# Performance work log

Hardware: AMD Instinct MI355X
Metric: run time of the kernel (lower is better)

Reference implementation:

```python
import jax, jax.numpy as jnp
import numpy as np

N = 50000      # nodes
E = 800000     # edges
F = 128        # node feature dim (= output_size, residual)
H = 128        # hidden_size

def _uniform_fan_avg(key, shape):
    # VarianceScaling(scale=1.0, mode='fan_avg', distribution='uniform')
    fan_avg = (shape[0] + shape[1]) / 2.0
    limit = np.sqrt(3.0 / fan_avg)
    return jax.random.uniform(key, shape, jnp.float32, -limit, limit)

def setup_inputs() -> dict:
    key = jax.random.key(0)
    ks = jax.random.split(key, 16)
    h = jax.random.normal(ks[0], (N, F), jnp.float32)
    pos = jax.random.normal(ks[1], (N, 3), jnp.float32)
    senders = jax.random.randint(ks[2], (E,), 0, N, jnp.int32)
    receivers = jax.random.randint(ks[3], (E,), 0, N, jnp.int32)
    # edge_mlp: Linear(2F+1 -> H) silu, Linear(H -> H) silu (activate_final=True)
    eW1 = _uniform_fan_avg(ks[4], (2 * F + 1, H)); eb1 = jnp.zeros((H,), jnp.float32)
    eW2 = _uniform_fan_avg(ks[5], (H, H)); eb2 = jnp.zeros((H,), jnp.float32)
    # node_mlp: Linear(F+H -> H) silu, Linear(H -> F) (no final act)
    nW1 = _uniform_fan_avg(ks[6], (F + H, H)); nb1 = jnp.zeros((H,), jnp.float32)
    nW2 = _uniform_fan_avg(ks[7], (H, F)); nb2 = jnp.zeros((F,), jnp.float32)
    # pos_correction_mlp: Linear(H -> H) silu, Linear(H -> 1, no bias, UniformScaling(dt))
    pW1 = _uniform_fan_avg(ks[8], (H, H)); pb1 = jnp.zeros((H,), jnp.float32)
    dt = 0.001
    pW2 = jax.random.uniform(ks[9], (H, 1), jnp.float32, -dt, dt) * np.sqrt(3.0)
    return {"h": h, "pos": pos, "senders": senders, "receivers": receivers,
            "eW1": eW1, "eb1": eb1, "eW2": eW2, "eb2": eb2,
            "nW1": nW1, "nb1": nb1, "nW2": nW2, "nb2": nb2,
            "pW1": pW1, "pb1": pb1, "pW2": pW2}

def reference(h, pos, senders, receivers,
              eW1, eb1, eW2, eb2,
              nW1, nb1, nW2, nb2,
              pW1, pb1, pW2):
    n = h.shape[0]
    # _coord2radial (normalize=False)
    coord_diff = pos[senders] - pos[receivers]            # [E,3]
    radial = jnp.sum(coord_diff ** 2, axis=1, keepdims=True)  # [E,1]
    # edge update (_message): concat(h[senders], h[receivers], radial) -> edge_mlp
    msg_in = jnp.concatenate([h[senders], h[receivers], radial], axis=-1)  # [E,2F+1]
    msg = jax.nn.silu(msg_in @ eW1 + eb1)
    msg = jax.nn.silu(msg @ eW2 + eb2)                    # [E,H]
    # node update (_update): aggregate messages at receivers, node_mlp, residual
    agg = jax.ops.segment_sum(msg, receivers, num_segments=n)  # [N,H]
    x = jnp.concatenate([h, agg], axis=-1)                # [N,F+H]
    x = jax.nn.silu(x @ nW1 + nb1)
    x = x @ nW2 + nb2                                     # [N,F]
    h_new = h + x                                         # residual
    # position update (_pos_update)
    pc = jax.nn.silu(msg @ pW1 + pb1) @ pW2               # [E,1]
    trans = jnp.clip(coord_diff * pc, -100, 100)          # [E,3]
    pos_new = pos + jax.ops.segment_sum(trans, senders, num_segments=n)
    return h_new, pos_new
```

## Files before the change

### kernel.cpp

```cpp
#include <hip/hip_runtime.h>
#include <hip/hip_bf16.h>

#define NNODES 50000
#define NEDGES 800000
#define EB 1024
#define SCAN_BLOCKS 196
#define TRN_BLOCKS 448

typedef short bf16x8 __attribute__((ext_vector_type(8)));
typedef float f32x4 __attribute__((ext_vector_type(4)));
typedef unsigned short u16;
typedef unsigned int u32;

__device__ __forceinline__ u16 f2bf(float f) {
    __hip_bfloat16 b = __float2bfloat16(f);
    return *reinterpret_cast<u16*>(&b);
}
__device__ __forceinline__ float bf2f(u16 v) {
    u32 u = ((u32)v) << 16;
    return __uint_as_float(u);
}
__device__ __forceinline__ u32 pack2(float a, float b) {
    __hip_bfloat162 t = __float22bfloat162_rn(float2{a, b});
    return *reinterpret_cast<u32*>(&t);
}
__device__ __forceinline__ float fast_silu(float x) {
    float e = __builtin_amdgcn_exp2f(-1.442695040888963f * x);
    return x * __builtin_amdgcn_rcpf(1.0f + e);
}
__device__ __forceinline__ bf16x8 ld8(const u16* p) {
    return *(const bf16x8*)p;
}
__device__ __forceinline__ f32x4 mfma16(bf16x8 a, bf16x8 b, f32x4 c) {
    return __builtin_amdgcn_mfma_f32_16x16x32_bf16(a, b, c, 0, 0, 0);
}
__device__ __forceinline__ void bar_lds() {
    asm volatile("s_waitcnt lgkmcnt(0)\n\ts_barrier" ::: "memory");
}

__global__ void prep_kernel(const float* __restrict__ eW1, const float* __restrict__ eW2,
                            const float* __restrict__ pW1, const float* __restrict__ nW1,
                            const float* __restrict__ nW2,
                            u16* __restrict__ eW1T, u16* __restrict__ eW2T,
                            u16* __restrict__ pW1T, u16* __restrict__ nW1T,
                            u16* __restrict__ nW2T,
                            const int* __restrict__ rcv, int* __restrict__ counts) {
    int b = blockIdx.x;
    if (b < TRN_BLOCKS) {
        int i = b * 256 + threadIdx.x;
        const float* src; u16* dst; int K;
        if (i < 32768)      { src = eW1; dst = eW1T; K = 256; }
        else if (i < 49152) { src = eW2; dst = eW2T; K = 128; i -= 32768; }
        else if (i < 65536) { src = pW1; dst = pW1T; K = 128; i -= 49152; }
        else if (i < 98304) { src = nW1; dst = nW1T; K = 256; i -= 65536; }
        else                { src = nW2; dst = nW2T; K = 128; i -= 98304; }
        int n = i / K, k = i - n * K;
        dst[i] = f2bf(src[k * 128 + n]);
    } else {
        int e = (b - TRN_BLOCKS) * 256 + threadIdx.x;
        if (e < NEDGES) atomicAdd(&counts[rcv[e]], 1);
    }
}

__global__ __launch_bounds__(256) void gemm_p(
    const float* __restrict__ h, const u16* __restrict__ eW1T,
    const u16* __restrict__ nW1T, const float* __restrict__ eb1,
    u16* __restrict__ P)
{
    const int tid  = threadIdx.x;
    const int w    = tid >> 6;
    const int lane = tid & 63;
    const int m    = lane & 15;
    const int quad = lane >> 4;
    const int ksub = quad * 8;

    bf16x8 bw[4][6];
    float bias[6];
    #pragma unroll
    for (int cc = 0; cc < 6; cc++) {
        int C = 96 * w + 16 * cc + m;
        const u16* bp;
        if (C < 128)      { bp = eW1T + C * 256;               bias[cc] = 0.5f * eb1[C]; }
        else if (C < 256) { bp = eW1T + (C - 128) * 256 + 128; bias[cc] = 0.5f * eb1[C - 128]; }
        else              { bp = nW1T + (C - 256) * 256;       bias[cc] = 0.f; }
        #pragma unroll
        for (int t = 0; t < 4; t++) bw[t][cc] = ld8(bp + t * 32 + ksub);
    }
    const int base = blockIdx.x * 64;
    #pragma unroll
    for (int mt = 0; mt < 4; mt++) {
        int nm = base + mt * 16 + m;
        if (nm >= NNODES) nm = NNODES - 1;
        bf16x8 afr[4];
        #pragma unroll
        for (int t = 0; t < 4; t++) {
            const float* ap = h + (size_t)nm * 128 + t * 32 + ksub;
            f32x4 lo = *(const f32x4*)ap;
            f32x4 hi = *(const f32x4*)(ap + 4);
            #pragma unroll
            for (int j = 0; j < 4; j++) {
                afr[t][j]     = (short)f2bf(lo[j]);
                afr[t][4 + j] = (short)f2bf(hi[j]);
            }
        }
        f32x4 acc[6];
        #pragma unroll
        for (int cc = 0; cc < 6; cc++) acc[cc] = (f32x4){0,0,0,0};
        #pragma unroll
        for (int t = 0; t < 4; t++)
            #pragma unroll
            for (int cc = 0; cc < 6; cc++)
                acc[cc] = mfma16(afr[t], bw[t][cc], acc[cc]);
        #pragma unroll
        for (int cc = 0; cc < 6; cc++) {
            int C = 96 * w + 16 * cc + m;
            #pragma unroll
            for (int r = 0; r < 4; r++) {
                int nr = base + mt * 16 + quad * 4 + r;
                if (nr < NNODES) P[(size_t)nr * 384 + C] = f2bf(acc[cc][r] + bias[cc]);
            }
        }
    }
}

__global__ void scan1(const int* __restrict__ counts, int* __restrict__ excl,
                      int* __restrict__ blkSum) {
    __shared__ int tmp[256];
    int tx = threadIdx.x;
    int i = blockIdx.x * 256 + tx;
    int v = (i < NNODES) ? counts[i] : 0;
    tmp[tx] = v;
    __syncthreads();
    for (int off = 1; off < 256; off <<= 1) {
        int t = (tx >= off) ? tmp[tx - off] : 0;
        __syncthreads();
        tmp[tx] += t;
        __syncthreads();
    }
    if (i < NNODES) excl[i] = tmp[tx] - v;
    if (tx == 255) blkSum[blockIdx.x] = tmp[255];
}
__global__ void scan2(const int* __restrict__ blkSum, int* __restrict__ blkOff) {
    __shared__ int tmp[256];
    int tx = threadIdx.x;
    int v = (tx < SCAN_BLOCKS) ? blkSum[tx] : 0;
    tmp[tx] = v;
    __syncthreads();
    for (int off = 1; off < 256; off <<= 1) {
        int t = (tx >= off) ? tmp[tx - off] : 0;
        __syncthreads();
        tmp[tx] += t;
        __syncthreads();
    }
    if (tx < SCAN_BLOCKS) blkOff[tx] = tmp[tx] - v;
}
__global__ void scan3(const int* __restrict__ excl, const int* __restrict__ blkOff,
                      int* __restrict__ cursor) {
    int i = blockIdx.x * 256 + threadIdx.x;
    if (i < NNODES) cursor[i] = excl[i] + blkOff[blockIdx.x];
}
__global__ void scatter_kernel(const int* __restrict__ rcv, int* __restrict__ cursor,
                               int* __restrict__ perm) {
    int e = blockIdx.x * 256 + threadIdx.x;
    if (e < NEDGES) {
        int p = atomicAdd(&cursor[rcv[e]], 1);
        perm[p] = e;
    }
}

struct __align__(16) EdgeLds {
    u16   m1[64 * 136];
    u16   msg[64 * 136];
    float diff[64][4];
    float pcpart[4][64];
    float wlast[128];
    int   sndloc[64];
    int   rcvloc[64];
    unsigned long long bmap;
};

__global__ __launch_bounds__(256, 4) void edge_kernel(
    const u16* __restrict__ P, const float* __restrict__ pos,
    const int* __restrict__ snd, const int* __restrict__ rcv,
    const int* __restrict__ perm,
    const float* __restrict__ eW1last,
    const u16* __restrict__ eW2T, const float* __restrict__ eb2,
    const u16* __restrict__ pW1T, const float* __restrict__ pb1,
    const float* __restrict__ pW2,
    float* __restrict__ agg, float* __restrict__ posacc)
{
    __shared__ EdgeLds S;
    const int tid  = threadIdx.x;
    const int w    = tid >> 6;
    const int lane = tid & 63;
    const int m    = lane & 15;
    const int quad = lane >> 4;
    const int ksub = quad * 8;

    bf16x8 bw2[4][2], bp1[4][2];
    float b2v[2], pb1v[2], pw2v[2];
    #pragma unroll
    for (int cc = 0; cc < 2; cc++) {
        int col = (2 * w + cc) * 16 + m;
        #pragma unroll
        for (int t = 0; t < 4; t++) {
            bw2[t][cc] = ld8(eW2T + col * 128 + t * 32 + ksub);
            bp1[t][cc] = ld8(pW1T + col * 128 + t * 32 + ksub);
        }
        b2v[cc]  = eb2[col];
        pb1v[cc] = pb1[col];
        pw2v[cc] = pW2[col];
    }
    if (tid < 128) S.wlast[tid] = eW1last[tid];

    const int NT  = NEDGES / 64;
    const int xcd = blockIdx.x & 7;
    const int ib  = blockIdx.x >> 3;
    const int per = (NT + 7) / 8;
    const int t0  = xcd * per;
    const int t1  = (t0 + per < NT) ? t0 + per : NT;

    int eg_n = 0, s_n = 0, r_n = 0;
    if (t0 + ib < t1) {
        eg_n = perm[(t0 + ib) * 64 + lane];
        s_n = snd[eg_n]; r_n = rcv[eg_n];
    }

    for (int t = t0 + ib; t < t1; t += 128) {
        const int s = s_n, r = r_n;
        const int tn = t + 128;
        const int tp = (tn < t1) ? tn : t;
        int eg2 = perm[tp * 64 + lane];

        float d0 = pos[s * 3 + 0] - pos[r * 3 + 0];
        float d1 = pos[s * 3 + 1] - pos[r * 3 + 1];
        float d2 = pos[s * 3 + 2] - pos[r * 3 + 2];
        float rad = d0 * d0 + d1 * d1 + d2 * d2;

        bar_lds();
        if (tid < 64) {
            S.sndloc[tid] = s; S.rcvloc[tid] = r;
            S.diff[tid][0] = d0; S.diff[tid][1] = d1; S.diff[tid][2] = d2;
            int pv = __shfl_up(r, 1);
            unsigned long long bm = __ballot(lane > 0 && r != pv);
            if (tid == 0) S.bmap = bm;
        }
        {
            const int sw = lane >> 3;
            const u16* pa = P + (size_t)s * 384 + w * 32;
            const u16* pb = P + (size_t)r * 384 + 128 + w * 32;
            #pragma unroll
            for (int k = 0; k < 4; k++) {
                bf16x8 va = ld8(pa + k * 8);
                bf16x8 vb = ld8(pb + k * 8);
                u32 pk[4];
                #pragma unroll
                for (int jj = 0; jj < 4; jj++) {
                    int col = w * 32 + k * 8 + jj * 2;
                    float2 wl = *(const float2*)&S.wlast[col];
                    float v0 = bf2f((u16)va[jj * 2])     + bf2f((u16)vb[jj * 2])     + rad * wl.x;
                    float v1 = bf2f((u16)va[jj * 2 + 1]) + bf2f((u16)vb[jj * 2 + 1]) + rad * wl.y;
                    pk[jj] = pack2(fast_silu(v0), fast_silu(v1));
                }
                int chunk = (w * 4 + k) ^ sw;
                *(uint4*)&S.m1[lane * 136 + chunk * 8] =
                    make_uint4(pk[0], pk[1], pk[2], pk[3]);
            }
        }
        s_n = snd[eg2]; r_n = rcv[eg2]; eg_n = eg2;

        bar_lds();
        #pragma unroll
        for (int mt = 0; mt < 4; mt++) {
            const int rs = mt * 2 + (m >> 3);
            const int row = mt * 16 + m;
            f32x4 acc0 = (f32x4){0,0,0,0}, acc1 = (f32x4){0,0,0,0};
            #pragma unroll
            for (int t4 = 0; t4 < 4; t4++) {
                bf16x8 a = *(const bf16x8*)&S.m1[row * 136 + ((t4 * 4 + quad) ^ rs) * 8];
                acc0 = mfma16(a, bw2[t4][0], acc0);
                acc1 = mfma16(a, bw2[t4][1], acc1);
            }
            #pragma unroll
            for (int cc = 0; cc < 2; cc++) {
                f32x4 acc = cc ? acc1 : acc0;
                int col = (2 * w + cc) * 16 + m;
                #pragma unroll
                for (int rr = 0; rr < 4; rr++) {
                    int orow = mt * 16 + quad * 4 + rr;
                    S.msg[orow * 136 + col] = f2bf(fast_silu(acc[rr] + b2v[cc]));
                }
            }
        }
        bar_lds();
        #pragma unroll
        for (int mt = 0; mt < 4; mt++) {
            f32x4 acc0 = (f32x4){0,0,0,0}, acc1 = (f32x4){0,0,0,0};
            #pragma unroll
            for (int t4 = 0; t4 < 4; t4++) {
                bf16x8 a = *(const bf16x8*)&S.msg[(mt * 16 + m) * 136 + t4 * 32 + ksub];
                acc0 = mfma16(a, bp1[t4][0], acc0);
                acc1 = mfma16(a, bp1[t4][1], acc1);
            }
            float p4[4];
            #pragma unroll
            for (int rr = 0; rr < 4; rr++)
                p4[rr] = fast_silu(acc0[rr] + pb1v[0]) * pw2v[0]
                       + fast_silu(acc1[rr] + pb1v[1]) * pw2v[1];
            #pragma unroll
            for (int mask = 1; mask < 16; mask <<= 1) {
                #pragma unroll
                for (int rr = 0; rr < 4; rr++) p4[rr] += __shfl_xor(p4[rr], mask);
            }
            if (m == 0) {
                #pragma unroll
                for (int rr = 0; rr < 4; rr++)
                    S.pcpart[w][mt * 16 + quad * 4 + rr] = p4[rr];
            }
        }
        {
            int half = tid >> 7, col = tid & 127;
            int r0 = half * 32;
            u32 bm32 = __builtin_amdgcn_readfirstlane((u32)(S.bmap >> r0)) & ~1u;
            float a = 0.f;
            int cur = S.rcvloc[r0];
            int rr = r0;
            const int end0 = r0 + 32;
            while (true) {
                int nb = bm32 ? (r0 + __builtin_ctz(bm32)) : end0;
                for (; rr < nb; ++rr) a += bf2f(S.msg[rr * 136 + col]);
                atomicAdd(&agg[(size_t)cur * 128 + col], a);
                if (nb == end0) break;
                a = 0.f;
                cur = S.rcvloc[nb];
                bm32 &= bm32 - 1;
            }
        }
        bar_lds();
        if (tid < 192) {
            int ee = tid / 3, c = tid - ee * 3;
            float pc = S.pcpart[0][ee] + S.pcpart[1][ee] + S.pcpart[2][ee] + S.pcpart[3][ee];
            float tr = S.diff[ee][c] * pc;
            tr = fminf(fmaxf(tr, -100.f), 100.f);
            atomicAdd(&posacc[S.sndloc[ee] * 3 + c], tr);
        }
    }
}

__global__ __launch_bounds__(256, 4) void node_kernel(
    const u16* __restrict__ P, const float* __restrict__ h,
    const float* __restrict__ agg,
    const u16* __restrict__ nW1T, const float* __restrict__ nb1,
    const u16* __restrict__ nW2T, const float* __restrict__ nb2,
    const float* __restrict__ pos, const float* __restrict__ posacc,
    float* __restrict__ out)
{
    __shared__ alignas(16) u16 m1[64 * 136];
    const int tid  = threadIdx.x;
    const int w    = tid >> 6;
    const int lane = tid & 63;
    const int m    = lane & 15;
    const int quad = lane >> 4;
    const int ksub = quad * 8;

    bf16x8 bw1[4][2], bw2[4][2];
    float b1v[2], b2v[2];
    #pragma unroll
    for (int cc = 0; cc < 2; cc++) {
        int col = (2 * w + cc) * 16 + m;
        #pragma unroll
        for (int t = 0; t < 4; t++) {
            bw1[t][cc] = ld8(nW1T + col * 256 + 128 + t * 32 + ksub);
            bw2[t][cc] = ld8(nW2T + col * 128 + t * 32 + ksub);
        }
        b1v[cc] = nb1[col];
        b2v[cc] = nb2[col];
    }
    const int base = blockIdx.x * 64;
    #pragma unroll
    for (int mt = 0; mt < 4; mt++) {
        int nm = base + mt * 16 + m;
        if (nm >= NNODES) nm = NNODES - 1;
        f32x4 acc0 = (f32x4){0,0,0,0}, acc1 = (f32x4){0,0,0,0};
        #pragma unroll
        for (int t = 0; t < 4; t++) {
            const float* ap = agg + (size_t)nm * 128 + t * 32 + ksub;
            f32x4 lo = *(const f32x4*)ap;
            f32x4 hi = *(const f32x4*)(ap + 4);
            bf16x8 a;
            #pragma unroll
            for (int j = 0; j < 4; j++) {
                a[j]     = (short)f2bf(lo[j]);
                a[4 + j] = (short)f2bf(hi[j]);
            }
            acc0 = mfma16(a, bw1[t][0], acc0);
            acc1 = mfma16(a, bw1[t][1], acc1);
        }
        #pragma unroll
        for (int cc = 0; cc < 2; cc++) {
            f32x4 acc = cc ? acc1 : acc0;
            int col = (2 * w + cc) * 16 + m;
            #pragma unroll
            for (int rr = 0; rr < 4; rr++) {
                int row = mt * 16 + quad * 4 + rr;
                int nrc = base + row; if (nrc >= NNODES) nrc = NNODES - 1;
                float v = acc[rr] + bf2f(P[(size_t)nrc * 384 + 256 + col]) + b1v[cc];
                m1[row * 136 + col] = f2bf(fast_silu(v));
            }
        }
    }
    __syncthreads();
    #pragma unroll
    for (int mt = 0; mt < 4; mt++) {
        f32x4 acc0 = (f32x4){0,0,0,0}, acc1 = (f32x4){0,0,0,0};
        #pragma unroll
        for (int t = 0; t < 4; t++) {
            bf16x8 a = *(const bf16x8*)&m1[(mt * 16 + m) * 136 + t * 32 + ksub];
            acc0 = mfma16(a, bw2[t][0], acc0);
            acc1 = mfma16(a, bw2[t][1], acc1);
        }
        #pragma unroll
        for (int cc = 0; cc < 2; cc++) {
            f32x4 acc = cc ? acc1 : acc0;
            int col = (2 * w + cc) * 16 + m;
            #pragma unroll
            for (int rr = 0; rr < 4; rr++) {
                int nr = base + mt * 16 + quad * 4 + rr;
                if (nr < NNODES)
                    out[(size_t)nr * 128 + col] = acc[rr] + b2v[cc] + h[(size_t)nr * 128 + col];
            }
        }
    }
    if (tid < 192) {
        int i = blockIdx.x * 192 + tid;
        if (i < NNODES * 3) out[NNODES * 128 + i] = pos[i] + posacc[i];
    }
}

extern "C" void kernel_launch(void* const* d_in, const int* in_sizes, int n_in,
                              void* d_out, int out_size, void* d_ws, size_t ws_size,
                              hipStream_t stream) {
    (void)in_sizes; (void)n_in; (void)out_size; (void)ws_size;
    const float* h   = (const float*)d_in[0];
    const float* pos = (const float*)d_in[1];
    const int*   snd = (const int*)d_in[2];
    const int*   rcv = (const int*)d_in[3];
    const float* eW1 = (const float*)d_in[4];
    const float* eb1 = (const float*)d_in[5];
    const float* eW2 = (const float*)d_in[6];
    const float* eb2 = (const float*)d_in[7];
    const float* nW1 = (const float*)d_in[8];
    const float* nb1 = (const float*)d_in[9];
    const float* nW2 = (const float*)d_in[10];
    const float* nb2 = (const float*)d_in[11];
    const float* pW1 = (const float*)d_in[12];
    const float* pb1 = (const float*)d_in[13];
    const float* pW2 = (const float*)d_in[14];
    float* out = (float*)d_out;

    float* agg    = (float*)d_ws;
    float* posacc = agg + (size_t)NNODES * 128;
    u16* P    = (u16*)(posacc + (size_t)NNODES * 3);
    u16* eW1T = P + (size_t)NNODES * 384;
    u16* eW2T = eW1T + 128 * 256;
    u16* pW1T = eW2T + 128 * 128;
    u16* nW1T = pW1T + 128 * 128;
    u16* nW2T = nW1T + 128 * 256;
    int* counts = (int*)(nW2T + 128 * 128);
    int* excl   = counts + 50048;
    int* blkSum = excl + 50048;
    int* blkOff = blkSum + 256;
    int* cursor = blkOff + 256;
    int* perm   = cursor + 50048;

    hipMemsetAsync(agg, 0, (size_t)NNODES * 131 * sizeof(float), stream);
    hipMemsetAsync(counts, 0, 50048 * sizeof(int), stream);

    prep_kernel<<<TRN_BLOCKS + (NEDGES + 255) / 256, 256, 0, stream>>>(
        eW1, eW2, pW1, nW1, nW2, eW1T, eW2T, pW1T, nW1T, nW2T, rcv, counts);

    gemm_p<<<(NNODES + 63) / 64, 256, 0, stream>>>(h, eW1T, nW1T, eb1, P);

    scan1<<<SCAN_BLOCKS, 256, 0, stream>>>(counts, excl, blkSum);
    scan2<<<1, 256, 0, stream>>>(blkSum, blkOff);
    scan3<<<SCAN_BLOCKS, 256, 0, stream>>>(excl, blkOff, cursor);
    scatter_kernel<<<(NEDGES + 255) / 256, 256, 0, stream>>>(rcv, cursor, perm);

    edge_kernel<<<EB, 256, 0, stream>>>(
        P, pos, snd, rcv, perm,
        eW1 + 256 * 128,
        eW2T, eb2, pW1T, pb1, pW2,
        agg, posacc);

    node_kernel<<<(NNODES + 63) / 64, 256, 0, stream>>>(
        P, h, agg, nW1T, nb1, nW2T, nb2, pos, posacc, out);
}
```

Before: 454.9 us.

## Swap MFMA operand order for packed msg stores and fold scan3 into scatter

```diff
diff --git a/kernel.cpp b/kernel.cpp
--- a/kernel.cpp
+++ b/kernel.cpp
@@ -154,16 +154,13 @@
     }
     if (tx < SCAN_BLOCKS) blkOff[tx] = tmp[tx] - v;
 }
-__global__ void scan3(const int* __restrict__ excl, const int* __restrict__ blkOff,
-                      int* __restrict__ cursor) {
-    int i = blockIdx.x * 256 + threadIdx.x;
-    if (i < NNODES) cursor[i] = excl[i] + blkOff[blockIdx.x];
-}
-__global__ void scatter_kernel(const int* __restrict__ rcv, int* __restrict__ cursor,
+__global__ void scatter_kernel(const int* __restrict__ rcv, const int* __restrict__ excl,
+                               const int* __restrict__ blkOff, int* __restrict__ delta,
                                int* __restrict__ perm) {
     int e = blockIdx.x * 256 + threadIdx.x;
     if (e < NEDGES) {
-        int p = atomicAdd(&cursor[rcv[e]], 1);
+        int r = rcv[e];
+        int p = excl[r] + blkOff[r >> 8] + atomicAdd(&delta[r], 1);
         perm[p] = e;
     }
 }
@@ -174,6 +171,9 @@
     float diff[64][4];
     float pcpart[4][64];
     float wlast[128];
+    float eb2s[128];
+    float pb1s[128];
+    float pw2s[128];
     int   sndloc[64];
     int   rcvloc[64];
     unsigned long long bmap;
@@ -198,7 +198,6 @@
     const int ksub = quad * 8;
 
     bf16x8 bw2[4][2], bp1[4][2];
-    float b2v[2], pb1v[2], pw2v[2];
     #pragma unroll
     for (int cc = 0; cc < 2; cc++) {
         int col = (2 * w + cc) * 16 + m;
@@ -207,11 +206,13 @@
             bw2[t][cc] = ld8(eW2T + col * 128 + t * 32 + ksub);
             bp1[t][cc] = ld8(pW1T + col * 128 + t * 32 + ksub);
         }
-        b2v[cc]  = eb2[col];
-        pb1v[cc] = pb1[col];
-        pw2v[cc] = pW2[col];
-    }
-    if (tid < 128) S.wlast[tid] = eW1last[tid];
+    }
+    if (tid < 128) {
+        S.wlast[tid] = eW1last[tid];
+        S.eb2s[tid]  = eb2[tid];
+        S.pb1s[tid]  = pb1[tid];
+        S.pw2s[tid]  = pW2[tid];
+    }
 
     const int NT  = NEDGES / 64;
     const int xcd = blockIdx.x & 7;
@@ -240,19 +241,20 @@
         bar_lds();
         if (tid < 64) {
             S.sndloc[tid] = s; S.rcvloc[tid] = r;
-            S.diff[tid][0] = d0; S.diff[tid][1] = d1; S.diff[tid][2] = d2;
+            S.diff[tid][0] = d0; S.diff[tid][1] = d1;
+            S.diff[tid][2] = d2; S.diff[tid][3] = 0.f;
             int pv = __shfl_up(r, 1);
             unsigned long long bm = __ballot(lane > 0 && r != pv);
             if (tid == 0) S.bmap = bm;
         }
         {
             const int sw = lane >> 3;
-            const u16* pa = P + (size_t)s * 384 + w * 32;
-            const u16* pb = P + (size_t)r * 384 + 128 + w * 32;
+            const u16* pap = P + (size_t)s * 384 + w * 32;
+            const u16* pbp = P + (size_t)r * 384 + 128 + w * 32;
             #pragma unroll
             for (int k = 0; k < 4; k++) {
-                bf16x8 va = ld8(pa + k * 8);
-                bf16x8 vb = ld8(pb + k * 8);
+                bf16x8 va = ld8(pap + k * 8);
+                bf16x8 vb = ld8(pbp + k * 8);
                 u32 pk[4];
                 #pragma unroll
                 for (int jj = 0; jj < 4; jj++) {
@@ -270,52 +272,52 @@
         s_n = snd[eg2]; r_n = rcv[eg2]; eg_n = eg2;
 
         bar_lds();
-        #pragma unroll
-        for (int mt = 0; mt < 4; mt++) {
-            const int rs = mt * 2 + (m >> 3);
-            const int row = mt * 16 + m;
-            f32x4 acc0 = (f32x4){0,0,0,0}, acc1 = (f32x4){0,0,0,0};
-            #pragma unroll
-            for (int t4 = 0; t4 < 4; t4++) {
-                bf16x8 a = *(const bf16x8*)&S.m1[row * 136 + ((t4 * 4 + quad) ^ rs) * 8];
-                acc0 = mfma16(a, bw2[t4][0], acc0);
-                acc1 = mfma16(a, bw2[t4][1], acc1);
-            }
-            #pragma unroll
-            for (int cc = 0; cc < 2; cc++) {
-                f32x4 acc = cc ? acc1 : acc0;
-                int col = (2 * w + cc) * 16 + m;
+        {
+            f32x4 b2a = *(const f32x4*)&S.eb2s[(2 * w + 0) * 16 + quad * 4];
+            f32x4 b2b = *(const f32x4*)&S.eb2s[(2 * w + 1) * 16 + quad * 4];
+            #pragma unroll
+            for (int mt = 0; mt < 4; mt++) {
+                const int rs = mt * 2 + (m >> 3);
+                const int row = mt * 16 + m;
+                f32x4 acc0 = (f32x4){0,0,0,0}, acc1 = (f32x4){0,0,0,0};
                 #pragma unroll
-                for (int rr = 0; rr < 4; rr++) {
-                    int orow = mt * 16 + quad * 4 + rr;
-                    S.msg[orow * 136 + col] = f2bf(fast_silu(acc[rr] + b2v[cc]));
+                for (int t4 = 0; t4 < 4; t4++) {
+                    bf16x8 a = *(const bf16x8*)&S.m1[row * 136 + ((t4 * 4 + quad) ^ rs) * 8];
+                    acc0 = mfma16(bw2[t4][0], a, acc0);
+                    acc1 = mfma16(bw2[t4][1], a, acc1);
                 }
+                u32 q0 = pack2(fast_silu(acc0[0] + b2a[0]), fast_silu(acc0[1] + b2a[1]));
+                u32 q1 = pack2(fast_silu(acc0[2] + b2a[2]), fast_silu(acc0[3] + b2a[3]));
+                u32 q2 = pack2(fast_silu(acc1[0] + b2b[0]), fast_silu(acc1[1] + b2b[1]));
+                u32 q3 = pack2(fast_silu(acc1[2] + b2b[2]), fast_silu(acc1[3] + b2b[3]));
+                *(uint2*)&S.msg[row * 136 + (2 * w + 0) * 16 + quad * 4] = make_uint2(q0, q1);
+                *(uint2*)&S.msg[row * 136 + (2 * w + 1) * 16 + quad * 4] = make_uint2(q2, q3);
             }
         }
         bar_lds();
-        #pragma unroll
-        for (int mt = 0; mt < 4; mt++) {
-            f32x4 acc0 = (f32x4){0,0,0,0}, acc1 = (f32x4){0,0,0,0};
-            #pragma unroll
-            for (int t4 = 0; t4 < 4; t4++) {
-                bf16x8 a = *(const bf16x8*)&S.msg[(mt * 16 + m) * 136 + t4 * 32 + ksub];
-                acc0 = mfma16(a, bp1[t4][0], acc0);
-                acc1 = mfma16(a, bp1[t4][1], acc1);
-            }
-            float p4[4];
-            #pragma unroll
-            for (int rr = 0; rr < 4; rr++)
-                p4[rr] = fast_silu(acc0[rr] + pb1v[0]) * pw2v[0]
-                       + fast_silu(acc1[rr] + pb1v[1]) * pw2v[1];
-            #pragma unroll
-            for (int mask = 1; mask < 16; mask <<= 1) {
+        {
+            f32x4 p1a = *(const f32x4*)&S.pb1s[(2 * w + 0) * 16 + quad * 4];
+            f32x4 p1b = *(const f32x4*)&S.pb1s[(2 * w + 1) * 16 + quad * 4];
+            f32x4 w2a = *(const f32x4*)&S.pw2s[(2 * w + 0) * 16 + quad * 4];
+            f32x4 w2b = *(const f32x4*)&S.pw2s[(2 * w + 1) * 16 + quad * 4];
+            #pragma unroll
+            for (int mt = 0; mt < 4; mt++) {
+                const int row = mt * 16 + m;
+                f32x4 acc0 = (f32x4){0,0,0,0}, acc1 = (f32x4){0,0,0,0};
                 #pragma unroll
-                for (int rr = 0; rr < 4; rr++) p4[rr] += __shfl_xor(p4[rr], mask);
-            }
-            if (m == 0) {
+                for (int t4 = 0; t4 < 4; t4++) {
+                    bf16x8 a = *(const bf16x8*)&S.msg[row * 136 + t4 * 32 + ksub];
+                    acc0 = mfma16(bp1[t4][0], a, acc0);
+                    acc1 = mfma16(bp1[t4][1], a, acc1);
+                }
+                float part = 0.f;
                 #pragma unroll
                 for (int rr = 0; rr < 4; rr++)
-                    S.pcpart[w][mt * 16 + quad * 4 + rr] = p4[rr];
+                    part += fast_silu(acc0[rr] + p1a[rr]) * w2a[rr]
+                          + fast_silu(acc1[rr] + p1b[rr]) * w2b[rr];
+                part += __shfl_xor(part, 16);
+                part += __shfl_xor(part, 32);
+                if (quad == 0) S.pcpart[w][mt * 16 + m] = part;
             }
         }
         {
@@ -467,14 +469,14 @@
     u16* nW1T = pW1T + 128 * 128;
     u16* nW2T = nW1T + 128 * 256;
     int* counts = (int*)(nW2T + 128 * 128);
-    int* excl   = counts + 50048;
+    int* delta  = counts + 50048;
+    int* excl   = delta + 50048;
     int* blkSum = excl + 50048;
     int* blkOff = blkSum + 256;
-    int* cursor = blkOff + 256;
-    int* perm   = cursor + 50048;
+    int* perm   = blkOff + 256;
 
     hipMemsetAsync(agg, 0, (size_t)NNODES * 131 * sizeof(float), stream);
-    hipMemsetAsync(counts, 0, 50048 * sizeof(int), stream);
+    hipMemsetAsync(counts, 0, 2 * 50048 * sizeof(int), stream);
 
     prep_kernel<<<TRN_BLOCKS + (NEDGES + 255) / 256, 256, 0, stream>>>(
         eW1, eW2, pW1, nW1, nW2, eW1T, eW2T, pW1T, nW1T, nW2T, rcv, counts);
@@ -483,8 +485,8 @@
 
     scan1<<<SCAN_BLOCKS, 256, 0, stream>>>(counts, excl, blkSum);
     scan2<<<1, 256, 0, stream>>>(blkSum, blkOff);
-    scan3<<<SCAN_BLOCKS, 256, 0, stream>>>(excl, blkOff, cursor);
-    scatter_kernel<<<(NEDGES + 255) / 256, 256, 0, stream>>>(rcv, cursor, perm);
+    scatter_kernel<<<(NEDGES + 255) / 256, 256, 0, stream>>>(
+        rcv, excl, blkOff, delta, perm);
 
     edge_kernel<<<EB, 256, 0, stream>>>(
         P, pos, snd, rcv, perm,
```

After: 460.1 us. About the same (+1.2%).
